# Optimization experiments

Measured on AMD Instinct MI355X. Metric: run time of the kernel, lower is better.

The kernel has to match this reference:

```python
import jax, jax.numpy as jnp
import numpy as np

INPUT_SIZE = 2048
HIDDEN_SIZE = 4096
NUM_CLASSES = 1000
BATCH = 4096


def setup_inputs() -> dict:
    key = jax.random.key(0)
    kx, k1, k2, k3 = jax.random.split(key, 4)
    x = jax.random.normal(kx, (BATCH, INPUT_SIZE), dtype=jnp.float32)
    w1 = jax.random.normal(k1, (INPUT_SIZE, HIDDEN_SIZE), dtype=jnp.float32) * 0.01
    b1 = jnp.zeros((HIDDEN_SIZE,), dtype=jnp.float32)
    w2 = jax.random.normal(k2, (HIDDEN_SIZE, HIDDEN_SIZE), dtype=jnp.float32) * 0.01
    b2 = jnp.zeros((HIDDEN_SIZE,), dtype=jnp.float32)
    w3 = jax.random.normal(k3, (HIDDEN_SIZE, NUM_CLASSES), dtype=jnp.float32) * 0.01
    b3 = jnp.zeros((NUM_CLASSES,), dtype=jnp.float32)
    return {"x": x, "w1": w1, "b1": b1, "w2": w2, "b2": b2, "w3": w3, "b3": b3}


def reference(x, w1, b1, w2, b2, w3, b3):
    # fused GEMM + bias + ReLU, equivalent to the original Python double-loop matmul
    h1 = jax.nn.relu(x @ w1 + b1)    # [B, H]
    h2 = jax.nn.relu(h1 @ w2 + b2)   # [B, H]
    out = h2 @ w3 + b3               # [B, C]
    return out
```

## Files before the change

kernel.cpp:

```cpp
#include <hip/hip_runtime.h>
#include <hip/hip_bf16.h>

typedef __bf16 bf16x8 __attribute__((ext_vector_type(8)));
typedef __bf16 bf16x4 __attribute__((ext_vector_type(4)));
typedef float floatx4 __attribute__((ext_vector_type(4)));

#define B_    4096
#define IN_   2048
#define HID_  4096
#define NC_   1000
#define NCP_  1024

__global__ __launch_bounds__(256) void cvt_f32_bf16(const float* __restrict__ src,
                                                    __bf16* __restrict__ dst, int n) {
    int i = (blockIdx.x * 256 + threadIdx.x) * 8;
    if (i + 7 < n) {
        float4 a = *(const float4*)(src + i);
        float4 b = *(const float4*)(src + i + 4);
        bf16x8 o;
        o[0] = (__bf16)a.x; o[1] = (__bf16)a.y; o[2] = (__bf16)a.z; o[3] = (__bf16)a.w;
        o[4] = (__bf16)b.x; o[5] = (__bf16)b.y; o[6] = (__bf16)b.z; o[7] = (__bf16)b.w;
        *(bf16x8*)(dst + i) = o;
    }
}

__global__ __launch_bounds__(256) void transpose_cvt(const float* __restrict__ src,
                                                     __bf16* __restrict__ dst,
                                                     int R, int C) {
    __shared__ float tile[64 * 65];
    const int r0 = blockIdx.x * 64;
    const int c0 = blockIdx.y * 64;
    const int t  = threadIdx.x;
#pragma unroll
    for (int it = 0; it < 4; ++it) {
        int lin = it * 256 + t;
        int sr = lin >> 4, c4 = lin & 15;
        int cb = c0 + c4 * 4;
        const float* s = src + (size_t)(r0 + sr) * C;
        float4 v;
        if (cb + 3 < C) {
            v = *(const float4*)(s + cb);
        } else {
            v.x = (cb + 0 < C) ? s[cb + 0] : 0.f;
            v.y = (cb + 1 < C) ? s[cb + 1] : 0.f;
            v.z = (cb + 2 < C) ? s[cb + 2] : 0.f;
            v.w = (cb + 3 < C) ? s[cb + 3] : 0.f;
        }
        tile[(c4 * 4 + 0) * 65 + sr] = v.x;
        tile[(c4 * 4 + 1) * 65 + sr] = v.y;
        tile[(c4 * 4 + 2) * 65 + sr] = v.z;
        tile[(c4 * 4 + 3) * 65 + sr] = v.w;
    }
    __syncthreads();
#pragma unroll
    for (int it = 0; it < 4; ++it) {
        int lin = it * 256 + t;
        int dr = lin >> 4, q4 = lin & 15;
        bf16x4 o;
#pragma unroll
        for (int j = 0; j < 4; ++j) o[j] = (__bf16)tile[dr * 65 + q4 * 4 + j];
        *(bf16x4*)(dst + (size_t)(c0 + dr) * R + r0 + q4 * 4) = o;
    }
}

template <bool RELU, bool OUT_BF16>
__global__ __launch_bounds__(256, 2) void gemm_bt(const __bf16* __restrict__ A,
                                                  const __bf16* __restrict__ Bt,
                                                  const float* __restrict__ bias,
                                                  void* __restrict__ Cv,
                                                  int M, int K, int Nstore) {
    __shared__ __bf16 sA[128 * 64];
    __shared__ __bf16 sB[128 * 64];

    const int tid   = threadIdx.x;
    const int lane  = tid & 63;
    const int wave  = tid >> 6;
    const int wr    = wave >> 1;
    const int wc    = wave & 1;
    const int mBase = blockIdx.y * 128;
    const int nBase = blockIdx.x * 128;
    const int lr    = lane >> 4;
    const int lc    = lane & 15;

    floatx4 acc[4][4];
#pragma unroll
    for (int i = 0; i < 4; ++i)
#pragma unroll
        for (int j = 0; j < 4; ++j) acc[i][j] = (floatx4)0.f;

    for (int k0 = 0; k0 < K; k0 += 64) {
#pragma unroll
        for (int it = 0; it < 4; ++it) {
            int lin = it * 256 + tid;
            int r   = lin >> 3;
            int kc  = (lin & 7) ^ (r & 7);
            const __bf16* ga = A  + (size_t)(mBase + r) * K + k0 + kc * 8;
            const __bf16* gb = Bt + (size_t)(nBase + r) * K + k0 + kc * 8;
            __builtin_amdgcn_global_load_lds(
                (__attribute__((address_space(1))) void*)ga,
                (__attribute__((address_space(3))) void*)(sA + lin * 8), 16, 0, 0);
            __builtin_amdgcn_global_load_lds(
                (__attribute__((address_space(1))) void*)gb,
                (__attribute__((address_space(3))) void*)(sB + lin * 8), 16, 0, 0);
        }
        __builtin_amdgcn_s_waitcnt(0);
        __syncthreads();

#pragma unroll
        for (int kk = 0; kk < 2; ++kk) {
            const int sw = (kk * 4 + lr) ^ (lc & 7);
            bf16x8 af[4], bfr[4];
#pragma unroll
            for (int i = 0; i < 4; ++i)
                af[i] = *(const bf16x8*)(sA + (wr * 64 + i * 16 + lc) * 64 + sw * 8);
#pragma unroll
            for (int j = 0; j < 4; ++j)
                bfr[j] = *(const bf16x8*)(sB + (wc * 64 + j * 16 + lc) * 64 + sw * 8);
#pragma unroll
            for (int i = 0; i < 4; ++i)
#pragma unroll
                for (int j = 0; j < 4; ++j)
                    acc[i][j] = __builtin_amdgcn_mfma_f32_16x16x32_bf16(af[i], bfr[j], acc[i][j], 0, 0, 0);
        }
        __syncthreads();
    }

#pragma unroll
    for (int j = 0; j < 4; ++j) {
        int col = nBase + wc * 64 + j * 16 + lc;
        if (col < Nstore) {
            float bv = bias[col];
#pragma unroll
            for (int i = 0; i < 4; ++i) {
                int rowb = mBase + wr * 64 + i * 16 + lr * 4;
#pragma unroll
                for (int r = 0; r < 4; ++r) {
                    float v = acc[i][j][r] + bv;
                    if (RELU) v = fmaxf(v, 0.f);
                    if (OUT_BF16)
                        ((__bf16*)Cv)[(size_t)(rowb + r) * Nstore + col] = (__bf16)v;
                    else
                        ((float*)Cv)[(size_t)(rowb + r) * Nstore + col] = v;
                }
            }
        }
    }
}

__global__ __launch_bounds__(256, 2) void gemm_sk(const __bf16* __restrict__ A,
                                                  const __bf16* __restrict__ Bt,
                                                  float* __restrict__ P,
                                                  int M, int KH, int Ktot) {
    __shared__ __bf16 sA[128 * 64];
    __shared__ __bf16 sB[128 * 64];

    const int tid   = threadIdx.x;
    const int lane  = tid & 63;
    const int wave  = tid >> 6;
    const int wr    = wave >> 1;
    const int wc    = wave & 1;
    const int mBase = blockIdx.y * 128;
    const int nBase = blockIdx.x * 128;
    const int z     = blockIdx.z;
    const int kOff  = z * KH;
    const int lr    = lane >> 4;
    const int lc    = lane & 15;

    floatx4 acc[4][4];
#pragma unroll
    for (int i = 0; i < 4; ++i)
#pragma unroll
        for (int j = 0; j < 4; ++j) acc[i][j] = (floatx4)0.f;

    for (int k0 = kOff; k0 < kOff + KH; k0 += 64) {
#pragma unroll
        for (int it = 0; it < 4; ++it) {
            int lin = it * 256 + tid;
            int r   = lin >> 3;
            int kc  = (lin & 7) ^ (r & 7);
            const __bf16* ga = A  + (size_t)(mBase + r) * Ktot + k0 + kc * 8;
            const __bf16* gb = Bt + (size_t)(nBase + r) * Ktot + k0 + kc * 8;
            __builtin_amdgcn_global_load_lds(
                (__attribute__((address_space(1))) void*)ga,
                (__attribute__((address_space(3))) void*)(sA + lin * 8), 16, 0, 0);
            __builtin_amdgcn_global_load_lds(
                (__attribute__((address_space(1))) void*)gb,
                (__attribute__((address_space(3))) void*)(sB + lin * 8), 16, 0, 0);
        }
        __builtin_amdgcn_s_waitcnt(0);
        __syncthreads();

#pragma unroll
        for (int kk = 0; kk < 2; ++kk) {
            const int sw = (kk * 4 + lr) ^ (lc & 7);
            bf16x8 af[4], bfr[4];
#pragma unroll
            for (int i = 0; i < 4; ++i)
                af[i] = *(const bf16x8*)(sA + (wr * 64 + i * 16 + lc) * 64 + sw * 8);
#pragma unroll
            for (int j = 0; j < 4; ++j)
                bfr[j] = *(const bf16x8*)(sB + (wc * 64 + j * 16 + lc) * 64 + sw * 8);
#pragma unroll
            for (int i = 0; i < 4; ++i)
#pragma unroll
                for (int j = 0; j < 4; ++j)
                    acc[i][j] = __builtin_amdgcn_mfma_f32_16x16x32_bf16(af[i], bfr[j], acc[i][j], 0, 0, 0);
        }
        __syncthreads();
    }

    float* Pz = P + (size_t)z * M * NCP_;
#pragma unroll
    for (int j = 0; j < 4; ++j) {
        int col = nBase + wc * 64 + j * 16 + lc;
#pragma unroll
        for (int i = 0; i < 4; ++i) {
            int rowb = mBase + wr * 64 + i * 16 + lr * 4;
#pragma unroll
            for (int r = 0; r < 4; ++r)
                Pz[(size_t)(rowb + r) * NCP_ + col] = acc[i][j][r];
        }
    }
}

__global__ __launch_bounds__(256) void reduce_bias(const float* __restrict__ P,
                                                   const float* __restrict__ b3,
                                                   float* __restrict__ out) {
    int c = blockIdx.x * 256 + threadIdx.x;
    int m = blockIdx.y;
    if (c < NC_)
        out[(size_t)m * NC_ + c] =
            P[(size_t)m * NCP_ + c] + P[(size_t)(B_ + m) * NCP_ + c] + b3[c];
}

extern "C" void kernel_launch(void* const* d_in, const int* in_sizes, int n_in,
                              void* d_out, int out_size, void* d_ws, size_t ws_size,
                              hipStream_t stream) {
    const float* x  = (const float*)d_in[0];
    const float* w1 = (const float*)d_in[1];
    const float* b1 = (const float*)d_in[2];
    const float* w2 = (const float*)d_in[3];
    const float* b2 = (const float*)d_in[4];
    const float* w3 = (const float*)d_in[5];
    const float* b3 = (const float*)d_in[6];
    float* out = (float*)d_out;

    char* ws = (char*)d_ws;
    __bf16* xb  = (__bf16*)(ws);
    __bf16* w1t = (__bf16*)(ws + (16u << 20));
    __bf16* w2t = (__bf16*)(ws + (32u << 20));
    __bf16* w3t = (__bf16*)(ws + (64u << 20));
    __bf16* h1  = (__bf16*)(ws + (72u << 20));
    __bf16* h2  = (__bf16*)(ws);
    float*  P   = (float*)(ws + (72u << 20));

    cvt_f32_bf16<<<(B_ * IN_) / 2048, 256, 0, stream>>>(x, xb, B_ * IN_);
    transpose_cvt<<<dim3(IN_ / 64, HID_ / 64), 256, 0, stream>>>(w1, w1t, IN_, HID_);
    transpose_cvt<<<dim3(HID_ / 64, HID_ / 64), 256, 0, stream>>>(w2, w2t, HID_, HID_);
    transpose_cvt<<<dim3(HID_ / 64, NCP_ / 64), 256, 0, stream>>>(w3, w3t, HID_, NC_);

    gemm_bt<true, true><<<dim3(HID_ / 128, B_ / 128), 256, 0, stream>>>(
        xb, w1t, b1, h1, B_, IN_, HID_);
    gemm_bt<true, true><<<dim3(HID_ / 128, B_ / 128), 256, 0, stream>>>(
        h1, w2t, b2, h2, B_, HID_, HID_);

    gemm_sk<<<dim3(NCP_ / 128, B_ / 128, 2), 256, 0, stream>>>(
        h2, w3t, P, B_, HID_ / 2, HID_);
    reduce_bias<<<dim3(NCP_ / 256, B_), 256, 0, stream>>>(P, b3, out);
}
```

Baseline: 427.7 us.

## Switch GEMMs to 32x32x16 MFMA, raise occupancy, use 4-way split-K for layer 3

Replaces the 16x16x32 bf16 MFMA tiling with 32x32x16 MFMA in both GEMM kernels. Each wave now holds 2x2 accumulators of 16 floats, so fewer LDS fragment reads are needed per MFMA. Launch bounds are raised to 4 blocks per SM to allow more occupancy. The final layer's split-K goes from 2 to 4 partitions, with partial results written into two workspace regions and summed in the reduce kernel. This adds partial-sum traffic and may raise register pressure under the tighter launch bound.

```diff
diff --git a/kernel.cpp b/kernel.cpp
--- a/kernel.cpp
+++ b/kernel.cpp
@@ -3,7 +3,7 @@
 
 typedef __bf16 bf16x8 __attribute__((ext_vector_type(8)));
 typedef __bf16 bf16x4 __attribute__((ext_vector_type(4)));
-typedef float floatx4 __attribute__((ext_vector_type(4)));
+typedef float floatx16 __attribute__((ext_vector_type(16)));
 
 #define B_    4096
 #define IN_   2048
@@ -64,7 +64,7 @@
 }
 
 template <bool RELU, bool OUT_BF16>
-__global__ __launch_bounds__(256, 2) void gemm_bt(const __bf16* __restrict__ A,
+__global__ __launch_bounds__(256, 4) void gemm_bt(const __bf16* __restrict__ A,
                                                   const __bf16* __restrict__ Bt,
                                                   const float* __restrict__ bias,
                                                   void* __restrict__ Cv,
@@ -79,14 +79,14 @@
     const int wc    = wave & 1;
     const int mBase = blockIdx.y * 128;
     const int nBase = blockIdx.x * 128;
-    const int lr    = lane >> 4;
-    const int lc    = lane & 15;
-
-    floatx4 acc[4][4];
-#pragma unroll
-    for (int i = 0; i < 4; ++i)
-#pragma unroll
-        for (int j = 0; j < 4; ++j) acc[i][j] = (floatx4)0.f;
+    const int l32   = lane & 31;
+    const int kh    = lane >> 5;
+
+    floatx16 acc[2][2];
+#pragma unroll
+    for (int i = 0; i < 2; ++i)
+#pragma unroll
+        for (int j = 0; j < 2; ++j) acc[i][j] = (floatx16)0.f;
 
     for (int k0 = 0; k0 < K; k0 += 64) {
 #pragma unroll
@@ -107,49 +107,56 @@
         __syncthreads();
 
 #pragma unroll
-        for (int kk = 0; kk < 2; ++kk) {
-            const int sw = (kk * 4 + lr) ^ (lc & 7);
-            bf16x8 af[4], bfr[4];
-#pragma unroll
-            for (int i = 0; i < 4; ++i)
-                af[i] = *(const bf16x8*)(sA + (wr * 64 + i * 16 + lc) * 64 + sw * 8);
-#pragma unroll
-            for (int j = 0; j < 4; ++j)
-                bfr[j] = *(const bf16x8*)(sB + (wc * 64 + j * 16 + lc) * 64 + sw * 8);
-#pragma unroll
-            for (int i = 0; i < 4; ++i)
-#pragma unroll
-                for (int j = 0; j < 4; ++j)
-                    acc[i][j] = __builtin_amdgcn_mfma_f32_16x16x32_bf16(af[i], bfr[j], acc[i][j], 0, 0, 0);
-        }
-        __syncthreads();
-    }
-
-#pragma unroll
-    for (int j = 0; j < 4; ++j) {
-        int col = nBase + wc * 64 + j * 16 + lc;
+        for (int kk = 0; kk < 4; ++kk) {
+            bf16x8 af[2], bfr[2];
+#pragma unroll
+            for (int i = 0; i < 2; ++i) {
+                int row = wr * 64 + i * 32 + l32;
+                int sw  = (kk * 2 + kh) ^ (row & 7);
+                af[i] = *(const bf16x8*)(sA + row * 64 + sw * 8);
+            }
+#pragma unroll
+            for (int j = 0; j < 2; ++j) {
+                int row = wc * 64 + j * 32 + l32;
+                int sw  = (kk * 2 + kh) ^ (row & 7);
+                bfr[j] = *(const bf16x8*)(sB + row * 64 + sw * 8);
+            }
+#pragma unroll
+            for (int i = 0; i < 2; ++i)
+#pragma unroll
+                for (int j = 0; j < 2; ++j)
+                    acc[i][j] = __builtin_amdgcn_mfma_f32_32x32x16_bf16(af[i], bfr[j], acc[i][j], 0, 0, 0);
+        }
+        __syncthreads();
+    }
+
+#pragma unroll
+    for (int j = 0; j < 2; ++j) {
+        int col = nBase + wc * 64 + j * 32 + l32;
         if (col < Nstore) {
             float bv = bias[col];
 #pragma unroll
-            for (int i = 0; i < 4; ++i) {
-                int rowb = mBase + wr * 64 + i * 16 + lr * 4;
-#pragma unroll
-                for (int r = 0; r < 4; ++r) {
+            for (int i = 0; i < 2; ++i) {
+                int rb = mBase + wr * 64 + i * 32 + kh * 4;
+#pragma unroll
+                for (int r = 0; r < 16; ++r) {
+                    int row = rb + (r & 3) + 8 * (r >> 2);
                     float v = acc[i][j][r] + bv;
                     if (RELU) v = fmaxf(v, 0.f);
                     if (OUT_BF16)
-                        ((__bf16*)Cv)[(size_t)(rowb + r) * Nstore + col] = (__bf16)v;
+                        ((__bf16*)Cv)[(size_t)row * Nstore + col] = (__bf16)v;
                     else
-                        ((float*)Cv)[(size_t)(rowb + r) * Nstore + col] = v;
+                        ((float*)Cv)[(size_t)row * Nstore + col] = v;
                 }
             }
         }
     }
 }
 
-__global__ __launch_bounds__(256, 2) void gemm_sk(const __bf16* __restrict__ A,
+__global__ __launch_bounds__(256, 4) void gemm_sk(const __bf16* __restrict__ A,
                                                   const __bf16* __restrict__ Bt,
-                                                  float* __restrict__ P,
+                                                  float* __restrict__ Plo,
+                                                  float* __restrict__ Phi,
                                                   int M, int KH, int Ktot) {
     __shared__ __bf16 sA[128 * 64];
     __shared__ __bf16 sB[128 * 64];
@@ -163,14 +170,14 @@
     const int nBase = blockIdx.x * 128;
     const int z     = blockIdx.z;
     const int kOff  = z * KH;
-    const int lr    = lane >> 4;
-    const int lc    = lane & 15;
-
-    floatx4 acc[4][4];
-#pragma unroll
-    for (int i = 0; i < 4; ++i)
-#pragma unroll
-        for (int j = 0; j < 4; ++j) acc[i][j] = (floatx4)0.f;
+    const int l32   = lane & 31;
+    const int kh    = lane >> 5;
+
+    floatx16 acc[2][2];
+#pragma unroll
+    for (int i = 0; i < 2; ++i)
+#pragma unroll
+        for (int j = 0; j < 2; ++j) acc[i][j] = (floatx16)0.f;
 
     for (int k0 = kOff; k0 < kOff + KH; k0 += 64) {
 #pragma unroll
@@ -191,46 +198,56 @@
         __syncthreads();
 
 #pragma unroll
-        for (int kk = 0; kk < 2; ++kk) {
-            const int sw = (kk * 4 + lr) ^ (lc & 7);
-            bf16x8 af[4], bfr[4];
-#pragma unroll
-            for (int i = 0; i < 4; ++i)
-                af[i] = *(const bf16x8*)(sA + (wr * 64 + i * 16 + lc) * 64 + sw * 8);
-#pragma unroll
-            for (int j = 0; j < 4; ++j)
-                bfr[j] = *(const bf16x8*)(sB + (wc * 64 + j * 16 + lc) * 64 + sw * 8);
-#pragma unroll
-            for (int i = 0; i < 4; ++i)
-#pragma unroll
-                for (int j = 0; j < 4; ++j)
-                    acc[i][j] = __builtin_amdgcn_mfma_f32_16x16x32_bf16(af[i], bfr[j], acc[i][j], 0, 0, 0);
-        }
-        __syncthreads();
-    }
-
-    float* Pz = P + (size_t)z * M * NCP_;
-#pragma unroll
-    for (int j = 0; j < 4; ++j) {
-        int col = nBase + wc * 64 + j * 16 + lc;
-#pragma unroll
-        for (int i = 0; i < 4; ++i) {
-            int rowb = mBase + wr * 64 + i * 16 + lr * 4;
-#pragma unroll
-            for (int r = 0; r < 4; ++r)
-                Pz[(size_t)(rowb + r) * NCP_ + col] = acc[i][j][r];
-        }
-    }
-}
-
-__global__ __launch_bounds__(256) void reduce_bias(const float* __restrict__ P,
+        for (int kk = 0; kk < 4; ++kk) {
+            bf16x8 af[2], bfr[2];
+#pragma unroll
+            for (int i = 0; i < 2; ++i) {
+                int row = wr * 64 + i * 32 + l32;
+                int sw  = (kk * 2 + kh) ^ (row & 7);
+                af[i] = *(const bf16x8*)(sA + row * 64 + sw * 8);
+            }
+#pragma unroll
+            for (int j = 0; j < 2; ++j) {
+                int row = wc * 64 + j * 32 + l32;
+                int sw  = (kk * 2 + kh) ^ (row & 7);
+                bfr[j] = *(const bf16x8*)(sB + row * 64 + sw * 8);
+            }
+#pragma unroll
+            for (int i = 0; i < 2; ++i)
+#pragma unroll
+                for (int j = 0; j < 2; ++j)
+                    acc[i][j] = __builtin_amdgcn_mfma_f32_32x32x16_bf16(af[i], bfr[j], acc[i][j], 0, 0, 0);
+        }
+        __syncthreads();
+    }
+
+    float* Pz = ((z < 2) ? Plo : Phi) + (size_t)(z & 1) * M * NCP_;
+#pragma unroll
+    for (int j = 0; j < 2; ++j) {
+        int col = nBase + wc * 64 + j * 32 + l32;
+#pragma unroll
+        for (int i = 0; i < 2; ++i) {
+            int rb = mBase + wr * 64 + i * 32 + kh * 4;
+#pragma unroll
+            for (int r = 0; r < 16; ++r) {
+                int row = rb + (r & 3) + 8 * (r >> 2);
+                Pz[(size_t)row * NCP_ + col] = acc[i][j][r];
+            }
+        }
+    }
+}
+
+__global__ __launch_bounds__(256) void reduce_bias(const float* __restrict__ Plo,
+                                                   const float* __restrict__ Phi,
                                                    const float* __restrict__ b3,
                                                    float* __restrict__ out) {
     int c = blockIdx.x * 256 + threadIdx.x;
     int m = blockIdx.y;
-    if (c < NC_)
-        out[(size_t)m * NC_ + c] =
-            P[(size_t)m * NCP_ + c] + P[(size_t)(B_ + m) * NCP_ + c] + b3[c];
+    if (c < NC_) {
+        size_t o = (size_t)m * NCP_ + c;
+        size_t s = (size_t)B_ * NCP_;
+        out[(size_t)m * NC_ + c] = Plo[o] + Plo[o + s] + Phi[o] + Phi[o + s] + b3[c];
+    }
 }
 
 extern "C" void kernel_launch(void* const* d_in, const int* in_sizes, int n_in,
@@ -252,7 +269,8 @@
     __bf16* w3t = (__bf16*)(ws + (64u << 20));
     __bf16* h1  = (__bf16*)(ws + (72u << 20));
     __bf16* h2  = (__bf16*)(ws);
-    float*  P   = (float*)(ws + (72u << 20));
+    float*  Plo = (float*)(ws + (32u << 20));
+    float*  Phi = (float*)(ws + (72u << 20));
 
     cvt_f32_bf16<<<(B_ * IN_) / 2048, 256, 0, stream>>>(x, xb, B_ * IN_);
     transpose_cvt<<<dim3(IN_ / 64, HID_ / 64), 256, 0, stream>>>(w1, w1t, IN_, HID_);
@@ -264,7 +282,7 @@
     gemm_bt<true, true><<<dim3(HID_ / 128, B_ / 128), 256, 0, stream>>>(
         h1, w2t, b2, h2, B_, HID_, HID_);
 
-    gemm_sk<<<dim3(NCP_ / 128, B_ / 128, 2), 256, 0, stream>>>(
-        h2, w3t, P, B_, HID_ / 2, HID_);
-    reduce_bias<<<dim3(NCP_ / 256, B_), 256, 0, stream>>>(P, b3, out);
-}
+    gemm_sk<<<dim3(NCP_ / 128, B_ / 128, 4), 256, 0, stream>>>(
+        h2, w3t, Plo, Phi, B_, HID_ / 4, HID_);
+    reduce_bias<<<dim3(NCP_ / 256, B_), 256, 0, stream>>>(Plo, Phi, b3, out);
+}
```

Result: slower. 461.6 us (+7.9%).
